# Kernel optimization log

Hardware: AMD Instinct MI355X
Metric: run time of the kernel (lower is better)

The kernel has to match this reference:

```python
import jax, jax.numpy as jnp
import numpy as np

# Config: B=4, S=2048, E=512, H=8 heads, D=E//H=64, FF=2048.
# QLayer (quantum circuit) is replaced by its linear stand-in matching the
# declared I/O dims: V: D->D per head, Q/K: D->1 (scalar per token).

EPS = 1e-5

def layernorm(x):
    # torch LayerNorm(elementwise_affine=False), population variance
    mu = jnp.mean(x, axis=-1, keepdims=True)
    var = jnp.var(x, axis=-1, keepdims=True)
    return (x - mu) / jnp.sqrt(var + EPS)


def setup_inputs() -> dict:
    key = jax.random.key(0)
    ks = jax.random.split(key, 12)
    B, S, E, H = 4, 2048, 512, 8
    D = E // H
    F = 2048
    u = lambda k, shape, fan: jax.random.uniform(k, shape, jnp.float32, -1.0 / np.sqrt(fan), 1.0 / np.sqrt(fan))
    return {
        "input1": jax.random.normal(ks[0], (B, S, E), jnp.float32),
        # per-head value projection D->D
        "Wv": u(ks[1], (H, D, D), D),
        "bv": u(ks[2], (H, D), D),
        # per-head scalar query / key projections D->1
        "Wq": u(ks[3], (H, D), D),
        "bq": u(ks[4], (H,), D),
        "Wk": u(ks[5], (H, D), D),
        "bk": u(ks[6], (H,), D),
        # merger MLP: E->F (GELU) -> E
        "W1": u(ks[7], (E, F), E),
        "b1": u(ks[8], (F,), E),
        "W2": u(ks[9], (F, E), F),
        "b2": u(ks[10], (E,), F),
    }


def reference(input1, Wv, bv, Wq, bq, Wk, bk, W1, b1, W2, b2):
    B, S, E = input1.shape
    H, D, _ = Wv.shape
    x = layernorm(input1)
    # chunk along last dim == reshape into heads
    xh = x.reshape(B, S, H, D)
    # per-head projections (vectorized over heads)
    V = jnp.einsum('bshd,hde->bshe', xh, Wv) + bv            # [B,S,H,D]
    Q = jnp.einsum('bshd,hd->bhs', xh, Wq) + bq[None, :, None]  # [B,H,S]
    K = jnp.einsum('bshd,hd->bhs', xh, Wk) + bk[None, :, None]  # [B,H,S]
    # quadratic-distance scores: A = -(Q - K)^2, [B,H,S,S]
    A = -jnp.square(Q[:, :, :, None] - K[:, :, None, :])
    attn = jax.nn.softmax(A * (1.0 / np.sqrt(D)), axis=-1)
    head_out = jnp.einsum('bhqk,bkhd->bqhd', attn, V).reshape(B, S, E)
    # merger: Linear -> GELU (exact) -> Linear, plus residual
    h = jax.nn.gelu(head_out @ W1 + b1, approximate=False)
    return h @ W2 + b2 + input1
```

## Files before the change

kernel.cpp:

```cpp
#include <hip/hip_runtime.h>
#include <hip/hip_bf16.h>


#define Bsz 4
#define Ssz 2048
#define Esz 512
#define Hsz 8
#define Dsz 64
#define Fsz 2048
#define NR 16

typedef __attribute__((ext_vector_type(8))) short bf16x8;
typedef __attribute__((ext_vector_type(4))) float f32x4;

__device__ __constant__ float RS[16] = {
    0.f, 1.0f, 0.70710678f, 0.57735027f, 0.5f, 0.44721360f, 0.40824829f,
    0.37796447f, 0.35355339f, 0.33333333f, 0.31622777f, 0.30151134f,
    0.28867513f, 0.27735010f, 0.26726124f, 0.25819889f};

static __device__ __forceinline__ void gload_lds16(const void* g, void* l) {
    __builtin_amdgcn_global_load_lds(
        (const __attribute__((address_space(1))) unsigned int*)g,
        (__attribute__((address_space(3))) unsigned int*)l, 16, 0, 0);
}

static __device__ __forceinline__ unsigned short f2bf(float f) {
    unsigned int b = __float_as_uint(f);
    b += 0x7FFFu + ((b >> 16) & 1u);
    return (unsigned short)(b >> 16);
}
static __device__ __forceinline__ float bf2f(unsigned short u) {
    return __int_as_float(((int)u) << 16);
}

__global__ __launch_bounds__(256) void prep_kernel(
    const float* __restrict__ x,
    const float* __restrict__ Wq, const float* __restrict__ bq,
    const float* __restrict__ Wk, const float* __restrict__ bk,
    const float* __restrict__ W1, const float* __restrict__ W2,
    float* __restrict__ Qo, float* __restrict__ Ko, __hip_bfloat16* __restrict__ Xn,
    __hip_bfloat16* __restrict__ W1T, __hip_bfloat16* __restrict__ W2T)
{
    int bid = blockIdx.x;
    if (bid < 2048) {
        int wid = threadIdx.x >> 6, lane = threadIdx.x & 63;
        int tok = bid * 4 + wid;
        int b = tok >> 11, s = tok & 2047;

        const float* xrow = x + (size_t)tok * Esz;
        float4 v0 = *(const float4*)&xrow[lane * 8];
        float4 v1 = *(const float4*)&xrow[lane * 8 + 4];

        float sum = v0.x + v0.y + v0.z + v0.w + v1.x + v1.y + v1.z + v1.w;
        #pragma unroll
        for (int off = 32; off > 0; off >>= 1) sum += __shfl_xor(sum, off);
        float mean = sum * (1.0f / 512.0f);

        float d[8] = {v0.x - mean, v0.y - mean, v0.z - mean, v0.w - mean,
                      v1.x - mean, v1.y - mean, v1.z - mean, v1.w - mean};
        float ss = 0.f;
        #pragma unroll
        for (int j = 0; j < 8; ++j) ss = fmaf(d[j], d[j], ss);
        #pragma unroll
        for (int off = 32; off > 0; off >>= 1) ss += __shfl_xor(ss, off);
        float inv = rsqrtf(ss * (1.0f / 512.0f) + 1e-5f);

        float xn[8];
        #pragma unroll
        for (int j = 0; j < 8; ++j) xn[j] = d[j] * inv;

        int h = lane >> 3, dsub = (lane & 7) * 8;
        union { bf16x8 v; unsigned short u[8]; } pk;
        #pragma unroll
        for (int j = 0; j < 8; ++j) pk.u[j] = f2bf(xn[j]);
        *(bf16x8*)((unsigned short*)Xn + (((size_t)(b * Hsz + h) * Ssz + s) * Dsz + dsub)) = pk.v;

        float4 wqa = *(const float4*)&Wq[h * 64 + dsub];
        float4 wqb = *(const float4*)&Wq[h * 64 + dsub + 4];
        float4 wka = *(const float4*)&Wk[h * 64 + dsub];
        float4 wkb = *(const float4*)&Wk[h * 64 + dsub + 4];
        float pq = xn[0]*wqa.x + xn[1]*wqa.y + xn[2]*wqa.z + xn[3]*wqa.w
                 + xn[4]*wqb.x + xn[5]*wqb.y + xn[6]*wqb.z + xn[7]*wqb.w;
        float pkv = xn[0]*wka.x + xn[1]*wka.y + xn[2]*wka.z + xn[3]*wka.w
                  + xn[4]*wkb.x + xn[5]*wkb.y + xn[6]*wkb.z + xn[7]*wkb.w;
        #pragma unroll
        for (int off = 1; off < 8; off <<= 1) {
            pq  += __shfl_xor(pq, off);
            pkv += __shfl_xor(pkv, off);
        }
        if ((lane & 7) == 0) {
            int bh = b * Hsz + h;
            Qo[bh * Ssz + s] = pq + bq[h];
            Ko[bh * Ssz + s] = pkv + bk[h];
        }
        return;
    }

    __shared__ float tile[32][33];
    const float* in;
    __hip_bfloat16* outp;
    int R, C, bx, by;
    if (bid < 3072) {
        int tb = bid - 2048;
        in = W1; outp = W1T; R = Esz; C = Fsz;
        bx = tb & 63; by = tb >> 6;
    } else {
        int tb = bid - 3072;
        in = W2; outp = W2T; R = Fsz; C = Esz;
        bx = tb & 15; by = tb >> 4;
    }
    int t = threadIdx.x;
    int tc = t & 31, tr = t >> 5;
    #pragma unroll
    for (int i = 0; i < 4; ++i) {
        int rr = by * 32 + tr + i * 8, cc = bx * 32 + tc;
        tile[tr + i * 8][tc] = in[(size_t)rr * C + cc];
    }
    __syncthreads();
    #pragma unroll
    for (int i = 0; i < 4; ++i) {
        int ro = bx * 32 + tr + i * 8, co = by * 32 + tc;
        outp[(size_t)ro * R + co] = __float2bfloat16(tile[tc][tr + i * 8]);
    }
}

__global__ __launch_bounds__(512) void attn_moments_block(
    const float* __restrict__ Kv, const __hip_bfloat16* __restrict__ Xn,
    const float* __restrict__ Wv, const float* __restrict__ bvp,
    float* __restrict__ M)
{
    int bh = blockIdx.x, h = bh & 7;
    int t = threadIdx.x;
    __shared__ float Wt[512][17];
    __shared__ float Gf[NR * 68];

    int w = t >> 6, lane = t & 63;
    int kk = lane >> 3, dg = lane & 7;
    int ng = w * 2;
    float acc[2][8] = {};
    float dacc[2] = {};

    const unsigned short* xb = (const unsigned short*)Xn + (size_t)bh * Ssz * Dsz + dg * 8;

    for (int c = 0; c < Ssz / 512; ++c) {
        int k0 = c * 512;
        float kv = Kv[bh * Ssz + k0 + t];
        float wn = __expf(-0.125f * kv * kv);
        float half = 0.5f * kv;
        __syncthreads();
        Wt[t][0] = wn;
        #pragma unroll
        for (int n = 1; n < NR; ++n) { wn *= half * RS[n]; Wt[t][n] = wn; }
        __syncthreads();

        for (int kc = 0; kc < 512 / 8; ++kc) {
            int kl = kc * 8 + kk;
            bf16x8 xv = *(const bf16x8*)&xb[(size_t)(k0 + kl) * Dsz];
            float xf[8];
            #pragma unroll
            for (int e = 0; e < 8; ++e) xf[e] = bf2f((unsigned short)xv[e]);
            #pragma unroll
            for (int n = 0; n < 2; ++n) {
                float wt = Wt[kl][ng + n];
                dacc[n] += wt;
                #pragma unroll
                for (int e = 0; e < 8; ++e) acc[n][e] = fmaf(wt, xf[e], acc[n][e]);
            }
        }
    }

    #pragma unroll
    for (int off = 8; off < 64; off <<= 1) {
        #pragma unroll
        for (int n = 0; n < 2; ++n) {
            dacc[n] += __shfl_xor(dacc[n], off);
            #pragma unroll
            for (int e = 0; e < 8; ++e) acc[n][e] += __shfl_xor(acc[n][e], off);
        }
    }
    if (lane < 8) {
        #pragma unroll
        for (int n = 0; n < 2; ++n) {
            float* gp = &Gf[(ng + n) * 68 + dg * 8];
            float4 lo = {acc[n][0], acc[n][1], acc[n][2], acc[n][3]};
            float4 hi = {acc[n][4], acc[n][5], acc[n][6], acc[n][7]};
            *(float4*)gp = lo;
            *(float4*)(gp + 4) = hi;
        }
    }
    if (lane == 0) {
        #pragma unroll
        for (int n = 0; n < 2; ++n) Gf[(ng + n) * 68 + 64] = dacc[n];
    }
    __syncthreads();

    #pragma unroll
    for (int rep = 0; rep < 2; ++rep) {
        int o = t + rep * 512;
        int n = o >> 6, dd = o & 63;
        float den = Gf[n * 68 + 64];
        float accv = den * bvp[h * 64 + dd];
        const float* wv = Wv + ((size_t)h * 64) * 64 + dd;
        #pragma unroll
        for (int e = 0; e < 64; ++e) accv = fmaf(Gf[n * 68 + e], wv[(size_t)e * 64], accv);
        M[(size_t)bh * NR * 68 + n * 68 + dd] = accv;
        if (dd == 0) M[(size_t)bh * NR * 68 + n * 68 + 64] = den;
    }
}

__global__ __launch_bounds__(256) void attn_apply(
    const float* __restrict__ Qv, const float* __restrict__ M, __hip_bfloat16* __restrict__ A1)
{
    int tok = blockIdx.x;
    int b = tok >> 11, s = tok & 2047;
    int t = threadIdx.x;
    #pragma unroll
    for (int rep = 0; rep < 2; ++rep) {
        int e = t + rep * 256;
        int h = e >> 6, dd = e & 63;
        int bh = b * 8 + h;
        float q = Qv[bh * Ssz + s];
        const float* Mb = M + (size_t)bh * NR * 68;
        float half = 0.5f * q;
        float phi = 1.0f;
        float num = Mb[dd], den = Mb[64];
        #pragma unroll
        for (int n = 1; n < NR; ++n) {
            phi *= half * RS[n];
            num = fmaf(phi, Mb[n * 68 + dd], num);
            den = fmaf(phi, Mb[n * 68 + 64], den);
        }
        A1[(size_t)tok * Esz + e] = __float2bfloat16(num / den);
    }
}

template <int KDIM, int NDIM, int BN, int EPI>
__global__ __launch_bounds__(256) void gemm_bf16(
    const __hip_bfloat16* __restrict__ A, const __hip_bfloat16* __restrict__ Bt,
    const float* __restrict__ bias, const float* __restrict__ resid,
    void* __restrict__ Out)
{
    constexpr int NT = KDIM / 32;
    constexpr int NWGX = NDIM / BN;
    constexpr int NWG = NWGX * 64;
    constexpr int FN = BN / 32;

    __shared__ unsigned short As[3][128][32];
    __shared__ unsigned short Bs[3][BN][32];

    int t = threadIdx.x;
    int w = t >> 6, lane = t & 63;
    int wr = w >> 1, wc = w & 1;

    int orig = blockIdx.x;
    int swz = (orig & 7) * (NWG / 8) + (orig >> 3);
    int bm = (swz / NWGX) * 128;
    int bn = (swz % NWGX) * BN;

    f32x4 acc[4][FN] = {};
    const int r = t >> 2, cg = (t & 3) * 8;

    auto stage = [&](int kt, int buf) {
        int k0 = kt * 32;
        gload_lds16(&A[(size_t)(bm + r) * KDIM + k0 + cg], &As[buf][r][cg]);
        gload_lds16(&A[(size_t)(bm + r + 64) * KDIM + k0 + cg], &As[buf][r + 64][cg]);
        gload_lds16(&Bt[(size_t)(bn + r) * KDIM + k0 + cg], &Bs[buf][r][cg]);
        if constexpr (BN == 128)
            gload_lds16(&Bt[(size_t)(bn + r + 64) * KDIM + k0 + cg], &Bs[buf][r + 64][cg]);
    };
    auto wait_stage = [&](bool more_inflight) {
        if (more_inflight) {
            if constexpr (BN == 128) asm volatile("s_waitcnt vmcnt(4)" ::: "memory");
            else                     asm volatile("s_waitcnt vmcnt(3)" ::: "memory");
        } else {
            asm volatile("s_waitcnt vmcnt(0)" ::: "memory");
        }
    };

    stage(0, 0);
    stage(1, 1);
    wait_stage(true);
    __builtin_amdgcn_s_barrier();
    __builtin_amdgcn_sched_barrier(0);

    for (int kt = 0; kt < NT; ++kt) {
        int cb = kt % 3;
        if (kt + 2 < NT) stage(kt + 2, (kt + 2) % 3);

        bf16x8 af[4], bfr[FN];
        #pragma unroll
        for (int i = 0; i < 4; ++i)
            af[i] = *(const bf16x8*)&As[cb][wr * 64 + i * 16 + (lane & 15)][(lane >> 4) * 8];
        #pragma unroll
        for (int j = 0; j < FN; ++j)
            bfr[j] = *(const bf16x8*)&Bs[cb][wc * (BN / 2) + j * 16 + (lane & 15)][(lane >> 4) * 8];
        #pragma unroll
        for (int i = 0; i < 4; ++i)
            #pragma unroll
            for (int j = 0; j < FN; ++j)
                acc[i][j] = __builtin_amdgcn_mfma_f32_16x16x32_bf16(af[i], bfr[j], acc[i][j], 0, 0, 0);

        if (kt + 1 < NT) {
            wait_stage(kt + 2 < NT);
            __builtin_amdgcn_s_barrier();
            __builtin_amdgcn_sched_barrier(0);
        }
    }

    int col0 = lane & 15, rowg = lane >> 4;
    #pragma unroll
    for (int i = 0; i < 4; ++i) {
        #pragma unroll
        for (int j = 0; j < FN; ++j) {
            #pragma unroll
            for (int v = 0; v < 4; ++v) {
                int m = bm + wr * 64 + i * 16 + rowg * 4 + v;
                int n = bn + wc * (BN / 2) + j * 16 + col0;
                float val = acc[i][j][v] + bias[n];
                if (EPI == 0) {
                    float g = 0.5f * val * (1.0f + erff(val * 0.70710678f));
                    ((__hip_bfloat16*)Out)[(size_t)m * NDIM + n] = __float2bfloat16(g);
                } else {
                    size_t idx = (size_t)m * NDIM + n;
                    ((float*)Out)[idx] = val + resid[idx];
                }
            }
        }
    }
}

extern "C" void kernel_launch(void* const* d_in, const int* in_sizes, int n_in,
                              void* d_out, int out_size, void* d_ws, size_t ws_size,
                              hipStream_t stream) {
    const float* x  = (const float*)d_in[0];
    const float* Wv = (const float*)d_in[1];
    const float* bv = (const float*)d_in[2];
    const float* Wq = (const float*)d_in[3];
    const float* bq = (const float*)d_in[4];
    const float* Wk = (const float*)d_in[5];
    const float* bk = (const float*)d_in[6];
    const float* W1 = (const float*)d_in[7];
    const float* b1 = (const float*)d_in[8];
    const float* W2 = (const float*)d_in[9];
    const float* b2 = (const float*)d_in[10];
    float* out = (float*)d_out;

    char* ws = (char*)d_ws;
    float* Qb    = (float*)(ws + 0);
    float* Kb    = (float*)(ws + 262144);
    __hip_bfloat16* Xn = (__hip_bfloat16*)(ws + 524288);
    __hip_bfloat16* A1 = (__hip_bfloat16*)(ws + 8912896);
    float* Mfull = (float*)(ws + 17301504);
    __hip_bfloat16* W1T  = (__hip_bfloat16*)(ws + 17441024);
    __hip_bfloat16* W2T  = (__hip_bfloat16*)(ws + 19538176);
    __hip_bfloat16* hbuf = (__hip_bfloat16*)(ws + 21635328);

    prep_kernel<<<dim3(4096), 256, 0, stream>>>(x, Wq, bq, Wk, bk, W1, W2, Qb, Kb, Xn, W1T, W2T);
    attn_moments_block<<<dim3(Bsz * Hsz), 512, 0, stream>>>(Kb, Xn, Wv, bv, Mfull);
    attn_apply<<<dim3(Bsz * Ssz), 256, 0, stream>>>(Qb, Mfull, A1);
    gemm_bf16<Esz, Fsz, 128, 0><<<dim3(1024), 256, 0, stream>>>(A1, W1T, b1, nullptr, hbuf);
    gemm_bf16<Fsz, Esz, 64, 1><<<dim3(512), 256, 0, stream>>>(hbuf, W2T, b2, x, out);
}
```

Baseline: 217.6 us.

## Retile bf16 GEMMs to 8 waves with XOR-swizzled LDS and deeper K tiles

The two MLP GEMMs now run with 512 threads (8 waves) per block instead of 256, with a templated warp layout and K-tile depth (BK=64 for the second GEMM). LDS tiles use an XOR swizzle on the 16-byte column slots to cut bank conflicts on the fragment reads. The goal is better latency hiding and fewer LDS stalls. The cost is smaller per-wave tiles, which means more fragment loads per MFMA, and vmcnt wait counts that must stay correct for each configuration.

```diff
diff --git a/kernel.cpp b/kernel.cpp
--- a/kernel.cpp
+++ b/kernel.cpp
@@ -234,44 +234,62 @@
     }
 }
 
-template <int KDIM, int NDIM, int BN, int EPI>
-__global__ __launch_bounds__(256) void gemm_bf16(
+template <int KDIM, int NDIM, int BN, int BK, int WRW, int EPI>
+__global__ __launch_bounds__(512, 4) void gemm_bf16(
     const __hip_bfloat16* __restrict__ A, const __hip_bfloat16* __restrict__ Bt,
     const float* __restrict__ bias, const float* __restrict__ resid,
     void* __restrict__ Out)
 {
-    constexpr int NT = KDIM / 32;
+    constexpr int NT = KDIM / BK;
+    constexpr int WCW = 8 / WRW;
+    constexpr int MROWS = 128 / WRW;
+    constexpr int MF = MROWS / 16;
+    constexpr int NCOLS = BN / WCW;
+    constexpr int NF = NCOLS / 16;
+    constexpr int KS = BK / 32;
+    constexpr int NSLOT = BK / 8;
+    constexpr int ACALLS = BK / 32;
+    constexpr int LPS = ACALLS + (BN * BK) / 4096;
     constexpr int NWGX = NDIM / BN;
     constexpr int NWG = NWGX * 64;
-    constexpr int FN = BN / 32;
-
-    __shared__ unsigned short As[3][128][32];
-    __shared__ unsigned short Bs[3][BN][32];
+
+    __shared__ unsigned short As[3][128][BK];
+    __shared__ unsigned short Bs[3][BN][BK];
 
     int t = threadIdx.x;
     int w = t >> 6, lane = t & 63;
-    int wr = w >> 1, wc = w & 1;
+    int wr = w / WCW, wc = w % WCW;
 
     int orig = blockIdx.x;
-    int swz = (orig & 7) * (NWG / 8) + (orig >> 3);
-    int bm = (swz / NWGX) * 128;
-    int bn = (swz % NWGX) * BN;
-
-    f32x4 acc[4][FN] = {};
-    const int r = t >> 2, cg = (t & 3) * 8;
+    int swzb = (orig & 7) * (NWG / 8) + (orig >> 3);
+    int bm = (swzb / NWGX) * 128;
+    int bn = (swzb % NWGX) * BN;
+
+    f32x4 acc[MF][NF] = {};
+
+    auto rswz = [](int r) -> int { return (BK == 32) ? ((r >> 1) & 3) : (r & 7); };
+
+    const int tr = t / NSLOT;
+    const int cgs = t & (NSLOT - 1);
 
     auto stage = [&](int kt, int buf) {
-        int k0 = kt * 32;
-        gload_lds16(&A[(size_t)(bm + r) * KDIM + k0 + cg], &As[buf][r][cg]);
-        gload_lds16(&A[(size_t)(bm + r + 64) * KDIM + k0 + cg], &As[buf][r + 64][cg]);
-        gload_lds16(&Bt[(size_t)(bn + r) * KDIM + k0 + cg], &Bs[buf][r][cg]);
-        if constexpr (BN == 128)
-            gload_lds16(&Bt[(size_t)(bn + r + 64) * KDIM + k0 + cg], &Bs[buf][r + 64][cg]);
+        int k0 = kt * BK;
+        #pragma unroll
+        for (int a = 0; a < ACALLS; ++a) {
+            int r = a * (4096 / BK) + tr;
+            int srcc = cgs ^ rswz(r);
+            gload_lds16(&A[(size_t)(bm + r) * KDIM + k0 + srcc * 8], &As[buf][r][cgs * 8]);
+        }
+        {
+            int r = tr;
+            int srcc = cgs ^ rswz(r);
+            gload_lds16(&Bt[(size_t)(bn + r) * KDIM + k0 + srcc * 8], &Bs[buf][r][cgs * 8]);
+        }
     };
     auto wait_stage = [&](bool more_inflight) {
         if (more_inflight) {
-            if constexpr (BN == 128) asm volatile("s_waitcnt vmcnt(4)" ::: "memory");
-            else                     asm volatile("s_waitcnt vmcnt(3)" ::: "memory");
+            if constexpr (LPS == 2) asm volatile("s_waitcnt vmcnt(2)" ::: "memory");
+            else                    asm volatile("s_waitcnt vmcnt(3)" ::: "memory");
         } else {
             asm volatile("s_waitcnt vmcnt(0)" ::: "memory");
         }
@@ -283,22 +301,38 @@
     __builtin_amdgcn_s_barrier();
     __builtin_amdgcn_sched_barrier(0);
 
+    const int l15 = lane & 15, lg = lane >> 4;
+
     for (int kt = 0; kt < NT; ++kt) {
         int cb = kt % 3;
         if (kt + 2 < NT) stage(kt + 2, (kt + 2) % 3);
 
-        bf16x8 af[4], bfr[FN];
-        #pragma unroll
-        for (int i = 0; i < 4; ++i)
-            af[i] = *(const bf16x8*)&As[cb][wr * 64 + i * 16 + (lane & 15)][(lane >> 4) * 8];
-        #pragma unroll
-        for (int j = 0; j < FN; ++j)
-            bfr[j] = *(const bf16x8*)&Bs[cb][wc * (BN / 2) + j * 16 + (lane & 15)][(lane >> 4) * 8];
-        #pragma unroll
-        for (int i = 0; i < 4; ++i)
-            #pragma unroll
-            for (int j = 0; j < FN; ++j)
-                acc[i][j] = __builtin_amdgcn_mfma_f32_16x16x32_bf16(af[i], bfr[j], acc[i][j], 0, 0, 0);
+        bf16x8 af[MF][KS], bfv[NF][KS];
+        #pragma unroll
+        for (int i = 0; i < MF; ++i) {
+            int rr = wr * MROWS + i * 16 + l15;
+            #pragma unroll
+            for (int ks = 0; ks < KS; ++ks) {
+                int slot = (lg + ks * 4) ^ rswz(rr);
+                af[i][ks] = *(const bf16x8*)&As[cb][rr][slot * 8];
+            }
+        }
+        #pragma unroll
+        for (int j = 0; j < NF; ++j) {
+            int rr = wc * NCOLS + j * 16 + l15;
+            #pragma unroll
+            for (int ks = 0; ks < KS; ++ks) {
+                int slot = (lg + ks * 4) ^ rswz(rr);
+                bfv[j][ks] = *(const bf16x8*)&Bs[cb][rr][slot * 8];
+            }
+        }
+        #pragma unroll
+        for (int i = 0; i < MF; ++i)
+            #pragma unroll
+            for (int j = 0; j < NF; ++j)
+                #pragma unroll
+                for (int ks = 0; ks < KS; ++ks)
+                    acc[i][j] = __builtin_amdgcn_mfma_f32_16x16x32_bf16(af[i][ks], bfv[j][ks], acc[i][j], 0, 0, 0);
 
         if (kt + 1 < NT) {
             wait_stage(kt + 2 < NT);
@@ -309,13 +343,13 @@
 
     int col0 = lane & 15, rowg = lane >> 4;
     #pragma unroll
-    for (int i = 0; i < 4; ++i) {
-        #pragma unroll
-        for (int j = 0; j < FN; ++j) {
+    for (int i = 0; i < MF; ++i) {
+        #pragma unroll
+        for (int j = 0; j < NF; ++j) {
             #pragma unroll
             for (int v = 0; v < 4; ++v) {
-                int m = bm + wr * 64 + i * 16 + rowg * 4 + v;
-                int n = bn + wc * (BN / 2) + j * 16 + col0;
+                int m = bm + wr * MROWS + i * 16 + rowg * 4 + v;
+                int n = bn + wc * NCOLS + j * 16 + col0;
                 float val = acc[i][j][v] + bias[n];
                 if (EPI == 0) {
                     float g = 0.5f * val * (1.0f + erff(val * 0.70710678f));
@@ -358,6 +392,6 @@
     prep_kernel<<<dim3(4096), 256, 0, stream>>>(x, Wq, bq, Wk, bk, W1, W2, Qb, Kb, Xn, W1T, W2T);
     attn_moments_block<<<dim3(Bsz * Hsz), 512, 0, stream>>>(Kb, Xn, Wv, bv, Mfull);
     attn_apply<<<dim3(Bsz * Ssz), 256, 0, stream>>>(Qb, Mfull, A1);
-    gemm_bf16<Esz, Fsz, 128, 0><<<dim3(1024), 256, 0, stream>>>(A1, W1T, b1, nullptr, hbuf);
-    gemm_bf16<Fsz, Esz, 64, 1><<<dim3(512), 256, 0, stream>>>(hbuf, W2T, b2, x, out);
-}
+    gemm_bf16<Esz, Fsz, 128, 32, 2, 0><<<dim3(1024), 512, 0, stream>>>(A1, W1T, b1, nullptr, hbuf);
+    gemm_bf16<Fsz, Esz, 64, 64, 4, 1><<<dim3(512), 512, 0, stream>>>(hbuf, W2T, b2, x, out);
+}
```

After: 195.9 us. -9.9%, faster.
